# Kernel tuning notes

Measured on AMD Instinct MI355X. Metric: run time of the kernel, lower is better.

The kernel has to match this reference:

```python
import jax, jax.numpy as jnp
import numpy as np

NEG = -9999.0
PAD_IDX = 0
SOS_IDX = 47


def setup_inputs() -> dict:
    key = jax.random.key(0)
    k1, k2, k3 = jax.random.split(key, 3)
    B, T, S = 1024, 512, 48
    features = jax.random.normal(k1, (B, T, S), dtype=jnp.float32)
    states = jax.random.randint(k2, (B, T), 1, S - 1)  # avoid pad/sos as gold tags
    mask = jnp.ones((B, T), dtype=jnp.float32)
    # transition matrix ~ N(-1, 0.1) with CRF structural constraints (as in __init__)
    transition = -1.0 + 0.1 * jax.random.normal(k3, (S, S), dtype=jnp.float32)
    transition = transition.at[SOS_IDX, :].set(NEG)
    transition = transition.at[:, PAD_IDX].set(NEG)
    transition = transition.at[PAD_IDX, :].set(NEG)
    transition = transition.at[PAD_IDX, PAD_IDX].set(0.0)
    return {"features": features, "states": states, "mask": mask, "transition": transition}


def _numerator(features, states, mask, transition):
    # score of the gold path: sum_t mask_t * (emission_t + transition[y_t, y_{t-1}])
    B = states.shape[0]
    sos_col = jnp.full((B, 1), SOS_IDX, dtype=states.dtype)
    states_ext = jnp.concatenate([sos_col, states], axis=1)  # [B, T+1]
    emis = jnp.take_along_axis(features, states[..., None], axis=2)[..., 0]  # [B, T]
    trans = transition[states_ext[:, 1:], states_ext[:, :-1]]  # [B, T]
    return jnp.sum((emis + trans) * mask, axis=1)  # [B]


def _denominator(features, mask, transition):
    # CRF forward algorithm: log-partition via log-sum-exp scan over time
    B, T, S = features.shape
    init = jnp.full((B, S), NEG, dtype=features.dtype).at[:, SOS_IDX].set(0.0)

    def step(score, xs):
        emis_t, mask_t = xs  # [B, S], [B]
        # new[b, i] = lse_j( score[b, j] + emis[b, i] + transition[i, j] )
        new = jax.nn.logsumexp(
            score[:, None, :] + emis_t[:, :, None] + transition[None, :, :], axis=-1
        )
        m = mask_t[:, None]
        return new * m + score * (1.0 - m), None

    final, _ = jax.lax.scan(
        step, init, (jnp.swapaxes(features, 0, 1), jnp.swapaxes(mask, 0, 1))
    )
    return jax.nn.logsumexp(final, axis=-1)  # [B]


def reference(features, states, mask, transition):
    numer = _numerator(features, states, mask, transition)
    denom = _denominator(features, mask, transition)
    # per-sequence negative log-likelihood (denominator - numerator)
    return denom - numer
```

## Files before the change

### kernel.cpp

```cpp
#include <hip/hip_runtime.h>
#include <math.h>

#define B 1024
#define T 512
#define S 48
#define SOS 47

__device__ __forceinline__ float rdlane1(float v) {
    return __int_as_float(__builtin_amdgcn_readlane(__float_as_int(v), 1));
}

__global__ __launch_bounds__(64, 1) void crf_fused(const float* __restrict__ feat,
                                                   const int* __restrict__ states,
                                                   const float* __restrict__ mask,
                                                   const float* __restrict__ trans,
                                                   float* __restrict__ out) {
    __shared__ __align__(16) float pbuf[2][64];
    const int b = blockIdx.x;
    const int lane = threadIdx.x;
    const int elane = (lane < S) ? lane : 0;
    const float* f_b = feat + (size_t)b * T * S;
    const float* m_b = mask + b * T;
    const int* st_b = states + b * T;

    float nsum = 0.f;
#pragma unroll
    for (int k2 = 0; k2 < T / 64; ++k2) {
        const int t = lane + k2 * 64;
        const int st = st_b[t];
        const int pv = (t == 0) ? SOS : st_b[t - 1];
        nsum += (f_b[t * S + st] + trans[st * S + pv]) * m_b[t];
    }

    float expT[S];
    {
        const float4* t4 = (const float4*)(trans + elane * S);
#pragma unroll
        for (int j4 = 0; j4 < S / 4; ++j4) {
            const float4 tv = t4[j4];
            expT[4 * j4 + 0] = (lane < S) ? __expf(tv.x) : 0.f;
            expT[4 * j4 + 1] = (lane < S) ? __expf(tv.y) : 0.f;
            expT[4 * j4 + 2] = (lane < S) ? __expf(tv.z) : 0.f;
            expT[4 * j4 + 3] = (lane < S) ? __expf(tv.w) : 0.f;
        }
    }

    float p = (lane == SOS) ? 1.f : 0.f;
    float M = 0.f;
    pbuf[0][lane] = p;

    float ering[8], mring[8];
#pragma unroll
    for (int k = 0; k < 8; ++k) {
        ering[k] = f_b[k * S + elane];
        mring[k] = m_b[k];
    }

#pragma unroll 1
    for (int tb = 0; tb < T / 8; ++tb) {
#pragma unroll
        for (int k = 0; k < 8; ++k) {
            const int t = tb * 8 + k;
            const float emis = ering[k];
            const float er = rdlane1(emis);
            const float E = __expf(emis - er);
            const float4* pb = (const float4*)pbuf[k & 1];
            float ax = 0.f, ay = 0.f, az = 0.f, aw = 0.f;
#pragma unroll
            for (int j4 = 0; j4 < S / 4; ++j4) {
                const float4 pv4 = pb[j4];
                ax = fmaf(expT[4 * j4 + 0], pv4.x, ax);
                ay = fmaf(expT[4 * j4 + 1], pv4.y, ay);
                az = fmaf(expT[4 * j4 + 2], pv4.z, az);
                aw = fmaf(expT[4 * j4 + 3], pv4.w, aw);
            }
            const float d = (ax + ay) + (az + aw);
            const float dr = rdlane1(d);
            const float rd = __builtin_amdgcn_rcpf(dr);
            const float pn = (d * rd) * E;
            const bool live = (mring[k] != 0.f);
            p = live ? pn : p;
            M = live ? (M + er + __logf(dr)) : M;
            pbuf[(k + 1) & 1][lane] = p;
            const int tp = (t + 8) & (T - 1);
            ering[k] = f_b[tp * S + elane];
            mring[k] = m_b[tp];
        }
    }

    float ps = p;
#pragma unroll
    for (int off = 32; off > 0; off >>= 1) {
        ps += __shfl_xor(ps, off, 64);
        nsum += __shfl_xor(nsum, off, 64);
    }
    if (lane == 0) out[b] = M + __logf(ps) - nsum;
}

extern "C" void kernel_launch(void* const* d_in, const int* in_sizes, int n_in,
                              void* d_out, int out_size, void* d_ws, size_t ws_size,
                              hipStream_t stream) {
    const float* feat   = (const float*)d_in[0];
    const int*   states = (const int*)d_in[1];
    const float* mask   = (const float*)d_in[2];
    const float* trans  = (const float*)d_in[3];
    float* out = (float*)d_out;

    crf_fused<<<dim3(B), dim3(64), 0, stream>>>(feat, states, mask, trans, out);
}
```

Baseline: 302.5 us.

## Defer normalization off the recurrence critical path and double-buffer emission prefetch

The step now writes the unnormalized product d*F to shared memory right away. The reciprocal and log of lane 1's sum are computed afterwards and applied one step later through the carried r_s/l_s factors, so readlane, rcp and log no longer sit between the dot product and the LDS store of the serial chain. Emission and mask prefetch now use a two-bank ring that loads the next block of 8 timesteps up front, the loop is unrolled by 2, and waves_per_eu(1) is set. This costs more registers and changes when the scaling is applied, which could shift numerical ranges slightly.

```diff
diff --git a/kernel.cpp b/kernel.cpp
--- a/kernel.cpp
+++ b/kernel.cpp
@@ -10,11 +10,13 @@
     return __int_as_float(__builtin_amdgcn_readlane(__float_as_int(v), 1));
 }
 
-__global__ __launch_bounds__(64, 1) void crf_fused(const float* __restrict__ feat,
-                                                   const int* __restrict__ states,
-                                                   const float* __restrict__ mask,
-                                                   const float* __restrict__ trans,
-                                                   float* __restrict__ out) {
+__global__ __launch_bounds__(64, 1)
+__attribute__((amdgpu_waves_per_eu(1)))
+void crf_fused(const float* __restrict__ feat,
+               const int* __restrict__ states,
+               const float* __restrict__ mask,
+               const float* __restrict__ trans,
+               float* __restrict__ out) {
     __shared__ __align__(16) float pbuf[2][64];
     const int b = blockIdx.x;
     const int lane = threadIdx.x;
@@ -45,50 +47,57 @@
         }
     }
 
-    float p = (lane == SOS) ? 1.f : 0.f;
+    float q = (lane == SOS) ? 1.f : 0.f;
     float M = 0.f;
-    pbuf[0][lane] = p;
+    float r_s = 1.f, l_s = 0.f;
+    pbuf[0][lane] = q;
 
-    float ering[8], mring[8];
+    float ering[2][8], mring[2][8];
 #pragma unroll
     for (int k = 0; k < 8; ++k) {
-        ering[k] = f_b[k * S + elane];
-        mring[k] = m_b[k];
+        ering[0][k] = f_b[k * S + elane];
+        mring[0][k] = m_b[k];
     }
 
-#pragma unroll 1
+#pragma unroll 2
     for (int tb = 0; tb < T / 8; ++tb) {
+        const int pb = tb & 1;
+        const int tn = ((tb + 1) & (T / 8 - 1)) * 8;
 #pragma unroll
         for (int k = 0; k < 8; ++k) {
-            const int t = tb * 8 + k;
-            const float emis = ering[k];
+            ering[pb ^ 1][k] = f_b[(tn + k) * S + elane];
+            mring[pb ^ 1][k] = m_b[tn + k];
+        }
+#pragma unroll
+        for (int k = 0; k < 8; ++k) {
+            const float emis = ering[pb][k];
             const float er = rdlane1(emis);
-            const float E = __expf(emis - er);
-            const float4* pb = (const float4*)pbuf[k & 1];
+            const float F = __expf(emis - er) * r_s;
+            const float4* qb = (const float4*)pbuf[k & 1];
             float ax = 0.f, ay = 0.f, az = 0.f, aw = 0.f;
 #pragma unroll
             for (int j4 = 0; j4 < S / 4; ++j4) {
-                const float4 pv4 = pb[j4];
+                const float4 pv4 = qb[j4];
                 ax = fmaf(expT[4 * j4 + 0], pv4.x, ax);
                 ay = fmaf(expT[4 * j4 + 1], pv4.y, ay);
                 az = fmaf(expT[4 * j4 + 2], pv4.z, az);
                 aw = fmaf(expT[4 * j4 + 3], pv4.w, aw);
             }
             const float d = (ax + ay) + (az + aw);
+            const float qn = d * F;
+            const bool live = (mring[pb][k] != 0.f);
+            q = live ? qn : q;
+            pbuf[(k + 1) & 1][lane] = q;
+            M = live ? (M + er + l_s) : M;
             const float dr = rdlane1(d);
-            const float rd = __builtin_amdgcn_rcpf(dr);
-            const float pn = (d * rd) * E;
-            const bool live = (mring[k] != 0.f);
-            p = live ? pn : p;
-            M = live ? (M + er + __logf(dr)) : M;
-            pbuf[(k + 1) & 1][lane] = p;
-            const int tp = (t + 8) & (T - 1);
-            ering[k] = f_b[tp * S + elane];
-            mring[k] = m_b[tp];
+            const float nl = __logf(dr);
+            const float nr = __builtin_amdgcn_rcpf(dr);
+            r_s = live ? nr : r_s;
+            l_s = live ? nl : l_s;
         }
     }
 
-    float ps = p;
+    float ps = q;
 #pragma unroll
     for (int off = 32; off > 0; off >>= 1) {
         ps += __shfl_xor(ps, off, 64);
```

After: 284.4 us. -6.0%, faster.

## Batch 16 sequences per wave and run CRF forward recurrence on bf16 MFMA

Applied to the files above, without the earlier changes.

Each wave now processes 16 sequences, computing the transition matrix-vector product for all of them with bf16 MFMA instructions through an LDS-staged probability matrix. Normalization switches from a per-step reciprocal and log to power-of-two exponent rescaling, with the log accumulated as exponent counts. The mask is precomputed into per-step bitmasks in shared memory. This cuts per-step scalar FMA work but reduces the grid to 64 blocks and introduces bf16 rounding of the recurrent state.

```diff
diff --git a/kernel.cpp b/kernel.cpp
--- a/kernel.cpp
+++ b/kernel.cpp
@@ -5,96 +5,165 @@
 #define T 512
 #define S 48
 #define SOS 47
+#define TS (T * S)
 
-__device__ __forceinline__ float rdlane1(float v) {
-    return __int_as_float(__builtin_amdgcn_readlane(__float_as_int(v), 1));
+typedef short short8 __attribute__((ext_vector_type(8)));
+typedef float f32x4 __attribute__((ext_vector_type(4)));
+
+__device__ __forceinline__ short f2bf(float f) {
+    unsigned u = __float_as_uint(f);
+    return (short)((u + 0x7FFFu + ((u >> 16) & 1u)) >> 16);
 }
 
-__global__ __launch_bounds__(64, 1) void crf_fused(const float* __restrict__ feat,
-                                                   const int* __restrict__ states,
-                                                   const float* __restrict__ mask,
-                                                   const float* __restrict__ trans,
-                                                   float* __restrict__ out) {
-    __shared__ __align__(16) float pbuf[2][64];
-    const int b = blockIdx.x;
+__global__ __launch_bounds__(64)
+__attribute__((amdgpu_waves_per_eu(1, 1)))
+void crf_mfma(const float* __restrict__ feat, const int* __restrict__ states,
+              const float* __restrict__ mask, const float* __restrict__ trans,
+              float* __restrict__ out) {
+    __shared__ __align__(16) short qlds[16 * 72];
+    __shared__ unsigned short m16[T];
+    __shared__ float nsum_l[16];
     const int lane = threadIdx.x;
-    const int elane = (lane < S) ? lane : 0;
-    const float* f_b = feat + (size_t)b * T * S;
-    const float* m_b = mask + b * T;
-    const int* st_b = states + b * T;
+    const int n = lane & 15, quad = lane >> 4;
+    const int b0 = blockIdx.x * 16;
 
-    float nsum = 0.f;
-#pragma unroll
-    for (int k2 = 0; k2 < T / 64; ++k2) {
-        const int t = lane + k2 * 64;
-        const int st = st_b[t];
-        const int pv = (t == 0) ? SOS : st_b[t - 1];
-        nsum += (f_b[t * S + st] + trans[st * S + pv]) * m_b[t];
+    {
+        const float* fr = feat + (size_t)(b0 + n) * TS;
+        const int* str = states + (b0 + n) * T;
+        const float* mr = mask + (b0 + n) * T;
+        float acc = 0.f;
+#pragma unroll 8
+        for (int k2 = 0; k2 < T / 4; ++k2) {
+            const int t = quad + 4 * k2;
+            const int st = str[t];
+            const int pv = (t == 0) ? SOS : str[t - 1];
+            const float m = mr[t];
+            acc += (fr[t * S + st] + trans[st * S + pv]) * m;
+            const unsigned long long bal = __ballot(m != 0.f);
+            if (lane < 4) m16[lane + 4 * k2] = (unsigned short)(bal >> (16 * lane));
+        }
+        acc += __shfl_xor(acc, 16, 64);
+        acc += __shfl_xor(acc, 32, 64);
+        if (quad == 0) nsum_l[n] = acc;
     }
 
-    float expT[S];
-    {
-        const float4* t4 = (const float4*)(trans + elane * S);
+    short8 Bf[3][2];
 #pragma unroll
-        for (int j4 = 0; j4 < S / 4; ++j4) {
-            const float4 tv = t4[j4];
-            expT[4 * j4 + 0] = (lane < S) ? __expf(tv.x) : 0.f;
-            expT[4 * j4 + 1] = (lane < S) ? __expf(tv.y) : 0.f;
-            expT[4 * j4 + 2] = (lane < S) ? __expf(tv.z) : 0.f;
-            expT[4 * j4 + 3] = (lane < S) ? __expf(tv.w) : 0.f;
+    for (int nt = 0; nt < 3; ++nt)
+#pragma unroll
+        for (int kc = 0; kc < 2; ++kc) {
+            short8 v;
+#pragma unroll
+            for (int e = 0; e < 8; ++e) {
+                const int k = kc * 32 + quad * 8 + e;
+                const float x = (k < S) ? __expf(trans[(nt * 16 + n) * S + k]) : 0.f;
+                v[e] = f2bf(x);
+            }
+            Bf[nt][kc] = v;
+        }
+
+    for (int i = lane; i < 16 * 72; i += 64) qlds[i] = 0;
+    if (lane < 16) qlds[lane * 72 + SOS] = (short)0x3F80;
+    float qreg[3][4];
+#pragma unroll
+    for (int nt = 0; nt < 3; ++nt)
+#pragma unroll
+        for (int r = 0; r < 4; ++r) qreg[nt][r] = 0.f;
+    if (n == 15)
+#pragma unroll
+        for (int r = 0; r < 4; ++r) qreg[2][r] = 1.f;
+
+    const float* rb[4];
+#pragma unroll
+    for (int r = 0; r < 4; ++r)
+        rb[r] = feat + (size_t)(b0 + quad * 4 + r) * TS + n;
+
+    float ering[4][12];
+#pragma unroll
+    for (int k = 0; k < 4; ++k)
+#pragma unroll
+        for (int nt = 0; nt < 3; ++nt)
+#pragma unroll
+            for (int r = 0; r < 4; ++r)
+                ering[k][nt * 4 + r] = rb[r][k * S + nt * 16];
+
+    const int a_base = n * 144 + quad * 16;
+    const int w_base = quad * 4 * 72 + n;
+    const int bp_addr = ((lane & 48) | 1) << 2;
+
+    float sc[4] = {1.f, 1.f, 1.f, 1.f};
+    float eexp[4] = {0.f, 0.f, 0.f, 0.f};
+    float Cc[4] = {0.f, 0.f, 0.f, 0.f};
+    const f32x4 zero4 = {0.f, 0.f, 0.f, 0.f};
+
+#pragma unroll 1
+    for (int tb = 0; tb < T / 4; ++tb) {
+#pragma unroll
+        for (int k = 0; k < 4; ++k) {
+            const int t = tb * 4 + k;
+            float E[12];
+#pragma unroll
+            for (int i = 0; i < 12; ++i) E[i] = __expf(ering[k][i]);
+            const int tp = (t + 4) & (T - 1);
+#pragma unroll
+            for (int nt = 0; nt < 3; ++nt)
+#pragma unroll
+                for (int r = 0; r < 4; ++r)
+                    ering[k][nt * 4 + r] = rb[r][tp * S + nt * 16];
+
+            const unsigned mm = m16[t];
+            const short8 a0 = *(const short8*)((const char*)qlds + a_base);
+            const short8 a1 = *(const short8*)((const char*)qlds + a_base + 64);
+
+            f32x4 d0 = __builtin_amdgcn_mfma_f32_16x16x32_bf16(a0, Bf[0][0], zero4, 0, 0, 0);
+            d0 = __builtin_amdgcn_mfma_f32_16x16x32_bf16(a1, Bf[0][1], d0, 0, 0, 0);
+            f32x4 d1 = __builtin_amdgcn_mfma_f32_16x16x32_bf16(a0, Bf[1][0], zero4, 0, 0, 0);
+            d1 = __builtin_amdgcn_mfma_f32_16x16x32_bf16(a1, Bf[1][1], d1, 0, 0, 0);
+            f32x4 d2 = __builtin_amdgcn_mfma_f32_16x16x32_bf16(a0, Bf[2][0], zero4, 0, 0, 0);
+            d2 = __builtin_amdgcn_mfma_f32_16x16x32_bf16(a1, Bf[2][1], d2, 0, 0, 0);
+            float dv[3][4];
+#pragma unroll
+            for (int r = 0; r < 4; ++r) { dv[0][r] = d0[r]; dv[1][r] = d1[r]; dv[2][r] = d2[r]; }
+
+            bool lv[4];
+#pragma unroll
+            for (int r = 0; r < 4; ++r)
+                lv[r] = ((mm >> (quad * 4 + r)) & 1u) != 0u;
+
+#pragma unroll
+            for (int nt = 0; nt < 3; ++nt)
+#pragma unroll
+                for (int r = 0; r < 4; ++r) {
+                    const float v = dv[nt][r] * E[nt * 4 + r] * sc[r];
+                    qreg[nt][r] = lv[r] ? v : qreg[nt][r];
+                    qlds[w_base + r * 72 + nt * 16] = f2bf(qreg[nt][r]);
+                }
+
+#pragma unroll
+            for (int r = 0; r < 4; ++r) {
+                Cc[r] += lv[r] ? eexp[r] * 0.69314718056f : 0.f;
+                const float dr = __int_as_float(
+                    __builtin_amdgcn_ds_bpermute(bp_addr, __float_as_int(qreg[0][r])));
+                int e = ((__float_as_int(dr) >> 23) & 0xFF) - 127;
+                e = min(12, max(-12, e));
+                eexp[r] = (float)e;
+                sc[r] = __int_as_float((unsigned)(127 - e) << 23);
+            }
         }
     }
 
-    float p = (lane == SOS) ? 1.f : 0.f;
-    float M = 0.f;
-    pbuf[0][lane] = p;
-
-    float ering[8], mring[8];
 #pragma unroll
-    for (int k = 0; k < 8; ++k) {
-        ering[k] = f_b[k * S + elane];
-        mring[k] = m_b[k];
-    }
-
-#pragma unroll 1
-    for (int tb = 0; tb < T / 8; ++tb) {
-#pragma unroll
-        for (int k = 0; k < 8; ++k) {
-            const int t = tb * 8 + k;
-            const float emis = ering[k];
-            const float er = rdlane1(emis);
-            const float E = __expf(emis - er);
-            const float4* pb = (const float4*)pbuf[k & 1];
-            float ax = 0.f, ay = 0.f, az = 0.f, aw = 0.f;
-#pragma unroll
-            for (int j4 = 0; j4 < S / 4; ++j4) {
-                const float4 pv4 = pb[j4];
-                ax = fmaf(expT[4 * j4 + 0], pv4.x, ax);
-                ay = fmaf(expT[4 * j4 + 1], pv4.y, ay);
-                az = fmaf(expT[4 * j4 + 2], pv4.z, az);
-                aw = fmaf(expT[4 * j4 + 3], pv4.w, aw);
-            }
-            const float d = (ax + ay) + (az + aw);
-            const float dr = rdlane1(d);
-            const float rd = __builtin_amdgcn_rcpf(dr);
-            const float pn = (d * rd) * E;
-            const bool live = (mring[k] != 0.f);
-            p = live ? pn : p;
-            M = live ? (M + er + __logf(dr)) : M;
-            pbuf[(k + 1) & 1][lane] = p;
-            const int tp = (t + 8) & (T - 1);
-            ering[k] = f_b[tp * S + elane];
-            mring[k] = m_b[tp];
+    for (int r = 0; r < 4; ++r) {
+        float s = qreg[0][r] + qreg[1][r] + qreg[2][r];
+        s += __shfl_xor(s, 1, 64);
+        s += __shfl_xor(s, 2, 64);
+        s += __shfl_xor(s, 4, 64);
+        s += __shfl_xor(s, 8, 64);
+        if (n == 0) {
+            const int row = quad * 4 + r;
+            out[b0 + row] = Cc[r] + __logf(s) - nsum_l[row];
         }
     }
-
-    float ps = p;
-#pragma unroll
-    for (int off = 32; off > 0; off >>= 1) {
-        ps += __shfl_xor(ps, off, 64);
-        nsum += __shfl_xor(nsum, off, 64);
-    }
-    if (lane == 0) out[b] = M + __logf(ps) - nsum;
 }
 
 extern "C" void kernel_launch(void* const* d_in, const int* in_sizes, int n_in,
@@ -106,5 +175,5 @@
     const float* trans  = (const float*)d_in[3];
     float* out = (float*)d_out;
 
-    crf_fused<<<dim3(B), dim3(64), 0, stream>>>(feat, states, mask, trans, out);
+    crf_mfma<<<dim3(B / 16), dim3(64), 0, stream>>>(feat, states, mask, trans, out);
 }
```

Result: slower. 519.6 us (+71.8%).
